# Performance work log

Measured on AMD Instinct MI355X. Metric: run time of the kernel, lower is better.

The kernel has to match this reference:

```python
import jax, jax.numpy as jnp
import numpy as np
from jax import lax


def _conv_block(x, w, b):
    # conv5x5 stride1 VALID + bias, ReLU, maxpool 2x2 stride 2 (NCHW)
    y = lax.conv_general_dilated(x, w, (1, 1), 'VALID',
                                 dimension_numbers=('NCHW', 'OIHW', 'NCHW'))
    y = jax.nn.relu(y + b[None, :, None, None])
    return lax.reduce_window(y, -np.inf, lax.max, (1, 1, 2, 2), (1, 1, 2, 2), 'VALID')


def _attention(feat, g, w, b):
    # feat: [B,C,H,W]; g: [B,512]; Linear(512 -> C)
    q = g @ w.T + b  # [B,C]
    Bn, C, H, W = feat.shape
    f = feat.reshape(Bn, C, H * W)
    # compat_scores[b,n] = sum_c f[b,c,n] * q[b,c] ; softmax over spatial dim
    a = jax.nn.softmax(jnp.einsum('bcn,bc->bn', f, q), axis=1)
    # weighted sum over spatial locations -> [B,C]
    return jnp.einsum('bcn,bn->bc', f, a)


def setup_inputs() -> dict:
    key = jax.random.key(0)
    ks = jax.random.split(key, 12)
    s = 0.02
    f32 = jnp.float32
    return {
        'x': jax.random.normal(ks[0], (16, 1, 220, 220), f32),
        'w1': jax.random.normal(ks[1], (64, 1, 5, 5), f32) * s,
        'b1': jnp.zeros((64,), f32),
        'w2': jax.random.normal(ks[2], (128, 64, 5, 5), f32) * s,
        'b2': jnp.zeros((128,), f32),
        'w3': jax.random.normal(ks[3], (256, 128, 5, 5), f32) * s,
        'b3': jnp.zeros((256,), f32),
        'fcw': jax.random.normal(ks[4], (512, 256 * 24 * 24), f32) * 0.002,
        'fcb': jnp.zeros((512,), f32),
        'aw1': jax.random.normal(ks[5], (64, 512), f32) * s,
        'ab1': jnp.zeros((64,), f32),
        'aw2': jax.random.normal(ks[6], (128, 512), f32) * s,
        'ab2': jnp.zeros((128,), f32),
        'aw3': jax.random.normal(ks[7], (256, 512), f32) * s,
        'ab3': jnp.zeros((256,), f32),
    }


def reference(x, w1, b1, w2, b2, w3, b3, fcw, fcb, aw1, ab1, aw2, ab2, aw3, ab3):
    o1 = _conv_block(x, w1, b1)    # [B,64,108,108]
    o2 = _conv_block(o1, w2, b2)   # [B,128,52,52]
    o3 = _conv_block(o2, w3, b3)   # [B,256,24,24]
    # dropout layers are identity at inference
    flat = o3.reshape(o3.shape[0], -1)          # [B, 256*24*24]
    g = flat @ fcw.T + fcb                       # [B, 512]
    att1 = _attention(o1, g, aw1, ab1)           # [B, 64]
    att2 = _attention(o2, g, aw2, ab2)           # [B, 128]
    att3 = _attention(o3, g, aw3, ab3)           # [B, 256]
    return jnp.concatenate([att1, att2, att3], axis=1)  # [B, 448]
```

## Files before the change

kernel.cpp:

```cpp
#include <hip/hip_runtime.h>
#include <cstdint>

typedef __attribute__((ext_vector_type(8))) short short8;
typedef __attribute__((ext_vector_type(4))) float f32x4;

__device__ __forceinline__ ushort f2bf(float f) {
  union { float f; uint32_t u; } v; v.f = f;
  uint32_t u = v.u;
  return (ushort)((u + 0x7fffu + ((u >> 16) & 1u)) >> 16);
}
__device__ __forceinline__ float bf2f(ushort h) {
  union { uint32_t u; float f; } v; v.u = ((uint32_t)h) << 16;
  return v.f;
}

__global__ __launch_bounds__(256) void prelude_k(
    const float* __restrict__ x, const float* __restrict__ w1, const float* __restrict__ b1,
    const float* __restrict__ w2, const float* __restrict__ w3,
    ushort* __restrict__ o1, ushort* __restrict__ w2t, ushort* __restrict__ w3t,
    float* __restrict__ g, float* __restrict__ out) {
  __shared__ ushort sb[28 * 29];
  const int tid = threadIdx.x;
  const int bx = blockIdx.x;
  if (bx >= 1296) {
    if (bx < 4496) {
      int idx = (bx - 1296) * 256 + tid;
      if (idx < 204800) {
        int j = idx & 7, lane = (idx >> 3) & 63, ks = (idx >> 9) & 1,
            fo = (idx >> 10) & 7, kpos = idx >> 13;
        int oc = fo * 16 + (lane & 15);
        int ic = ks * 32 + (lane >> 4) * 8 + j;
        w2t[idx] = f2bf(w2[((size_t)oc * 64 + ic) * 25 + kpos]);
      }
      {
        int j = idx & 7, lane = (idx >> 3) & 63, ks = (idx >> 9) & 3,
            fo = (idx >> 11) & 15, kpos = idx >> 15;
        int oc = fo * 16 + (lane & 15);
        int ic = ks * 32 + (lane >> 4) * 8 + j;
        w3t[idx] = f2bf(w3[((size_t)oc * 128 + ic) * 25 + kpos]);
      }
    } else {
      for (int i = tid; i < 8192; i += 256) g[i] = 0.f;
      for (int i = tid; i < 7168; i += 256) out[i] = 0.f;
    }
    return;
  }
  const int b = bx / 81, rem = bx % 81, ty = rem / 9, tx = rem % 9;
  for (int i = tid; i < 784; i += 256) {
    int iy = i / 28, ix = i % 28;
    sb[iy * 29 + ix] = f2bf(x[((size_t)b * 220 + ty * 24 + iy) * 220 + tx * 24 + ix]);
  }
  __syncthreads();
  const int lane = tid & 63, wid = tid >> 6;
  const int m16 = lane & 15, qd = lane >> 4;
  short8 bfr[4];
#pragma unroll
  for (int n = 0; n < 4; n++) {
    union { ushort u[8]; short8 v; } t;
#pragma unroll
    for (int j = 0; j < 8; j++) {
      int k = qd * 8 + j;
      int kc = k < 25 ? k : 0;
      ushort val = f2bf(w1[(n * 16 + m16) * 25 + kc]);
      t.u[j] = (k < 25) ? val : (ushort)0;
    }
    bfr[n] = t.v;
  }
  int offs[8];
#pragma unroll
  for (int j = 0; j < 8; j++) {
    int k = qd * 8 + j;
    int kc = k < 25 ? k : 24;
    offs[j] = (kc / 5) * 29 + (kc % 5);
  }
  float bias[4];
#pragma unroll
  for (int n = 0; n < 4; n++) bias[n] = b1[n * 16 + m16];
  for (int gg = 0; gg < 9; gg++) {
    int gr = wid * 9 + gg;
    int wglob = gr * 4 + (m16 >> 2);
    int wy = wglob / 12, wx = wglob % 12;
    int py = wy * 2 + ((m16 >> 1) & 1), px = wx * 2 + (m16 & 1);
    int base = py * 29 + px;
    union { ushort u[8]; short8 v; } a;
#pragma unroll
    for (int j = 0; j < 8; j++) a.u[j] = sb[base + offs[j]];
    int wgd = gr * 4 + qd;
    int gy = ty * 12 + wgd / 12, gx = tx * 12 + wgd % 12;
    size_t oidx = (((size_t)b * 108 + gy) * 108 + gx) * 64;
#pragma unroll
    for (int n = 0; n < 4; n++) {
      f32x4 d = (f32x4){0.f, 0.f, 0.f, 0.f};
      d = __builtin_amdgcn_mfma_f32_16x16x32_bf16(a.v, bfr[n], d, 0, 0, 0);
      float mx = fmaxf(fmaxf(d[0], d[1]), fmaxf(d[2], d[3]));
      o1[oidx + n * 16 + m16] = f2bf(fmaxf(mx + bias[n], 0.f));
    }
  }
}

template <int IC, int ICP, int OCT, int OCB, int INW, int POOLW>
__global__ __launch_bounds__(256) void conv_mfma(const ushort* __restrict__ in,
                                                 const ushort* __restrict__ wt,
                                                 const float* __restrict__ bias,
                                                 ushort* __restrict__ out) {
  constexpr int NPIX = 144;
  constexpr int PSTRIDE = OCB + 8;
  constexpr int LDSA = 2 * NPIX * ICP;
  constexpr int LDSP = 2 * 64 * PSTRIDE;
  constexpr int LDSN = (LDSA > LDSP) ? LDSA : LDSP;
  constexpr int NKS = IC / 32;
  constexpr int NFRAG = OCT / 16;
  __shared__ ushort sm[LDSN];
  const int tid = threadIdx.x;
  const int wid = tid >> 6, lane = tid & 63;
  const int m16 = lane & 15, qd = lane >> 4;
  const int bh = wid >> 1, og = wid & 1;
  constexpr int OCSPLIT = OCT / OCB;
  const int bpair = blockIdx.z / OCSPLIT;
  const int ocblk = (blockIdx.z % OCSPLIT) * OCB;
  const int b0 = bpair * 2;
  const int ty = blockIdx.y, tx = blockIdx.x;
  {
    constexpr int C8 = IC / 8;
    for (int i = tid; i < 2 * NPIX * C8; i += 256) {
      int bb = i / (NPIX * C8), rem = i % (NPIX * C8);
      int px = rem / C8, c8 = rem % C8;
      int gy = ty * 8 + px / 12, gx = tx * 8 + px % 12;
      uint4 v = *(const uint4*)(in + (((size_t)(b0 + bb) * INW + gy) * INW + gx) * IC + c8 * 8);
      *(uint4*)&sm[(bb * NPIX + px) * ICP + c8 * 8] = v;
    }
  }
  __syncthreads();
  f32x4 acc[4][4];
#pragma unroll
  for (int i = 0; i < 4; i++)
#pragma unroll
    for (int j = 0; j < 4; j++) acc[i][j] = (f32x4){0.f, 0.f, 0.f, 0.f};
  int aoff[4];
#pragma unroll
  for (int ms = 0; ms < 4; ms++) {
    int p = ms * 16 + m16;
    aoff[ms] = (bh * NPIX + (p >> 3) * 12 + (p & 7)) * ICP + qd * 8;
  }
  const int fo0 = (ocblk >> 4) + og * 4;
  for (int ky = 0; ky < 5; ky++) {
#pragma unroll
    for (int kx = 0; kx < 5; kx++) {
      const int koff = (ky * 12 + kx) * ICP;
      const ushort* wkp = wt + (((size_t)(ky * 5 + kx) * NFRAG + fo0) * NKS) * 512 + lane * 8;
#pragma unroll
      for (int ks = 0; ks < NKS; ks++) {
        short8 afr[4], bfr[4];
#pragma unroll
        for (int ms = 0; ms < 4; ms++)
          afr[ms] = *(const short8*)&sm[aoff[ms] + koff + ks * 32];
#pragma unroll
        for (int ns = 0; ns < 4; ns++)
          bfr[ns] = *(const short8*)(wkp + (ns * NKS + ks) * 512);
#pragma unroll
        for (int ms = 0; ms < 4; ms++)
#pragma unroll
          for (int ns = 0; ns < 4; ns++)
            acc[ms][ns] = __builtin_amdgcn_mfma_f32_16x16x32_bf16(afr[ms], bfr[ns], acc[ms][ns], 0, 0, 0);
      }
    }
  }
  __syncthreads();
#pragma unroll
  for (int ms = 0; ms < 4; ms++)
#pragma unroll
    for (int ns = 0; ns < 4; ns++) {
      int ocl = og * 64 + ns * 16 + m16;
      float bv = bias[ocblk + ocl];
#pragma unroll
      for (int r = 0; r < 4; r++) {
        int p = ms * 16 + qd * 4 + r;
        sm[(bh * 64 + p) * PSTRIDE + ocl] = f2bf(fmaxf(acc[ms][ns][r] + bv, 0.f));
      }
    }
  __syncthreads();
  constexpr int OC2 = OCB / 2;
  const int oc2 = tid % OC2, pst = tid / OC2;
  for (int pp = pst; pp < 32; pp += 256 / OC2) {
    int bb = pp >> 4, pl = pp & 15;
    int ppy = pl >> 2, ppx = pl & 3;
    int p00 = (ppy * 2) * 8 + ppx * 2;
    int oc = oc2 * 2;
    int base = bb * 64 * PSTRIDE;
    uint32_t v0 = *(const uint32_t*)&sm[base + p00 * PSTRIDE + oc];
    uint32_t v1 = *(const uint32_t*)&sm[base + (p00 + 1) * PSTRIDE + oc];
    uint32_t v2 = *(const uint32_t*)&sm[base + (p00 + 8) * PSTRIDE + oc];
    uint32_t v3 = *(const uint32_t*)&sm[base + (p00 + 9) * PSTRIDE + oc];
    float a0 = fmaxf(fmaxf(bf2f(v0 & 0xffff), bf2f(v1 & 0xffff)),
                     fmaxf(bf2f(v2 & 0xffff), bf2f(v3 & 0xffff)));
    float a1 = fmaxf(fmaxf(bf2f(v0 >> 16), bf2f(v1 >> 16)),
                     fmaxf(bf2f(v2 >> 16), bf2f(v3 >> 16)));
    uint32_t packed = ((uint32_t)f2bf(a1) << 16) | (uint32_t)f2bf(a0);
    int gy = ty * 4 + ppy, gx = tx * 4 + ppx;
    *(uint32_t*)&out[(((size_t)(b0 + bb) * POOLW + gy) * POOLW + gx) * OCT + ocblk + oc] = packed;
  }
}

__global__ void transpose_o3(const ushort* __restrict__ o3, ushort* __restrict__ flatT) {
  __shared__ ushort t[32][33];
  const int b = blockIdx.z;
  const int n0 = blockIdx.x * 32, c0 = blockIdx.y * 32;
  const int tid = threadIdx.x;
  {
    int cl = tid & 31, r = tid >> 5;
    for (int i = 0; i < 4; i++) {
      int nl = r + i * 8;
      t[nl][cl] = o3[((size_t)b * 576 + n0 + nl) * 256 + c0 + cl];
    }
  }
  __syncthreads();
  {
    int nl = tid & 31, r = tid >> 5;
    for (int i = 0; i < 4; i++) {
      int cl = r + i * 8;
      flatT[(size_t)b * 147456 + (c0 + cl) * 576 + n0 + nl] = t[nl][cl];
    }
  }
}

__global__ void fc_mfma(const ushort* __restrict__ flatT, const float* __restrict__ fcw,
                        float* __restrict__ g) {
  const int tid = threadIdx.x;
  const int wid = tid >> 6, lane = tid & 63;
  const int m16 = lane & 15, qd = lane >> 4;
  const int jt = blockIdx.y * 256 + wid * 64;
  const int K0 = blockIdx.x * 576;
  f32x4 acc[4];
#pragma unroll
  for (int f = 0; f < 4; f++) acc[f] = (f32x4){0.f, 0.f, 0.f, 0.f};
  const ushort* ap = flatT + (size_t)m16 * 147456 + K0 + qd * 8;
  const float* bp = fcw + (size_t)(jt + m16) * 147456 + K0 + qd * 8;
#pragma unroll 2
  for (int ks = 0; ks < 18; ks++) {
    short8 a = *(const short8*)(ap + ks * 32);
#pragma unroll
    for (int f = 0; f < 4; f++) {
      const float* bpf = bp + (size_t)f * 16 * 147456 + ks * 32;
      float4 b0 = *(const float4*)bpf;
      float4 b1 = *(const float4*)(bpf + 4);
      short8 bb;
      bb[0] = (short)f2bf(b0.x); bb[1] = (short)f2bf(b0.y);
      bb[2] = (short)f2bf(b0.z); bb[3] = (short)f2bf(b0.w);
      bb[4] = (short)f2bf(b1.x); bb[5] = (short)f2bf(b1.y);
      bb[6] = (short)f2bf(b1.z); bb[7] = (short)f2bf(b1.w);
      acc[f] = __builtin_amdgcn_mfma_f32_16x16x32_bf16(a, bb, acc[f], 0, 0, 0);
    }
  }
  const int brow = qd * 4;
#pragma unroll
  for (int f = 0; f < 4; f++)
#pragma unroll
    for (int r = 0; r < 4; r++)
      atomicAdd(&g[(brow + r) * 512 + jt + f * 16 + m16], acc[f][r]);
}

__global__ __launch_bounds__(256) void qcalc(const float* __restrict__ g,
                                             const float* __restrict__ fcb,
                                             const float* __restrict__ aw1, const float* __restrict__ ab1,
                                             const float* __restrict__ aw2, const float* __restrict__ ab2,
                                             const float* __restrict__ aw3, const float* __restrict__ ab3,
                                             float* __restrict__ q) {
  const int b = blockIdx.x, tid = threadIdx.x;
  __shared__ float gs[512];
  for (int i = tid; i < 512; i += 256) gs[i] = g[b * 512 + i] + fcb[i];
  __syncthreads();
  for (int c = tid; c < 448; c += 256) {
    const float* ar;
    float acc;
    if (c < 64)       { ar = aw1 + (size_t)c * 512;         acc = ab1[c]; }
    else if (c < 192) { ar = aw2 + (size_t)(c - 64) * 512;  acc = ab2[c - 64]; }
    else              { ar = aw3 + (size_t)(c - 192) * 512; acc = ab3[c - 192]; }
#pragma unroll 4
    for (int j = 0; j < 512; j += 4) {
      float4 a4 = *(const float4*)(ar + j);
      acc += a4.x * gs[j] + a4.y * gs[j + 1] + a4.z * gs[j + 2] + a4.w * gs[j + 3];
    }
    q[b * 448 + c] = acc;
  }
}

template <int C, int COFF>
__device__ __forceinline__ void score_head(const ushort* __restrict__ f,
                                           const float* __restrict__ q,
                                           float* __restrict__ s, int N, int nblk, int b,
                                           float* sq) {
  const int tid = threadIdx.x;
  if (tid < C) sq[tid] = q[b * 448 + COFF + tid];
  __syncthreads();
  int n = nblk * 256 + tid;
  if (n >= N) return;
  const ushort* fr = f + ((size_t)b * N + n) * C;
  float acc = 0.f;
#pragma unroll
  for (int c0 = 0; c0 < C; c0 += 8) {
    uint4 v = *(const uint4*)&fr[c0];
    uint32_t arr[4] = {v.x, v.y, v.z, v.w};
#pragma unroll
    for (int k = 0; k < 4; k++) {
      acc += bf2f(arr[k] & 0xffff) * sq[c0 + 2 * k];
      acc += bf2f(arr[k] >> 16) * sq[c0 + 2 * k + 1];
    }
  }
  s[(size_t)b * N + n] = acc;
}

__global__ void scores_all(const ushort* __restrict__ o1, const ushort* __restrict__ o2,
                           const ushort* __restrict__ o3, const float* __restrict__ q,
                           float* __restrict__ s1, float* __restrict__ s2,
                           float* __restrict__ s3) {
  __shared__ float sq[256];
  const int bx = blockIdx.x, b = blockIdx.y;
  if (bx < 46)      score_head<64, 0>(o1, q, s1, 11664, bx, b, sq);
  else if (bx < 57) score_head<128, 64>(o2, q, s2, 2704, bx - 46, b, sq);
  else              score_head<256, 192>(o3, q, s3, 576, bx - 57, b, sq);
}

__global__ void stats_all(const float* __restrict__ s1, const float* __restrict__ s2,
                          const float* __restrict__ s3, float* __restrict__ st) {
  const int b = blockIdx.x, head = blockIdx.y, tid = threadIdx.x;
  const float* s; int N; float* stp;
  if (head == 0)      { s = s1; N = 11664; stp = st; }
  else if (head == 1) { s = s2; N = 2704;  stp = st + 32; }
  else                { s = s3; N = 576;   stp = st + 64; }
  const float* sb = s + (size_t)b * N;
  __shared__ float red[4];
  float m = -1e30f;
  for (int i = tid; i < N; i += 256) m = fmaxf(m, sb[i]);
  for (int o = 32; o; o >>= 1) m = fmaxf(m, __shfl_xor(m, o));
  if ((tid & 63) == 0) red[tid >> 6] = m;
  __syncthreads();
  m = fmaxf(fmaxf(red[0], red[1]), fmaxf(red[2], red[3]));
  __syncthreads();
  float l = 0.f;
  for (int i = tid; i < N; i += 256) l += __expf(sb[i] - m);
  for (int o = 32; o; o >>= 1) l += __shfl_xor(l, o);
  if ((tid & 63) == 0) red[tid >> 6] = l;
  __syncthreads();
  if (tid == 0) { stp[b * 2] = m; stp[b * 2 + 1] = red[0] + red[1] + red[2] + red[3]; }
}

template <int C, int COFF, int CHUNK>
__device__ __forceinline__ void wsum_head(const ushort* __restrict__ f,
                                          const float* __restrict__ s,
                                          const float* __restrict__ st,
                                          float* __restrict__ out, int N, int nblk, int b) {
  const int tid = threadIdx.x;
  constexpr int S = 256 / C;
  const int c = tid % C, sub = tid / C;
  const float m = st[b * 2], rl = 1.f / st[b * 2 + 1];
  const float* sb = s + (size_t)b * N;
  const ushort* fb = f + (size_t)b * N * C;
  int n0 = nblk * CHUNK;
  int n1 = n0 + CHUNK; if (n1 > N) n1 = N;
  float acc = 0.f;
  for (int n = n0 + sub; n < n1; n += S) {
    float w = __expf(sb[n] - m);
    acc += w * bf2f(fb[(size_t)n * C + c]);
  }
  atomicAdd(&out[b * 448 + COFF + c], acc * rl);
}

__global__ void wsum_all(const ushort* __restrict__ o1, const ushort* __restrict__ o2,
                         const ushort* __restrict__ o3, const float* __restrict__ s1,
                         const float* __restrict__ s2, const float* __restrict__ s3,
                         const float* __restrict__ st, float* __restrict__ out) {
  const int bx = blockIdx.x, b = blockIdx.y;
  if (bx < 24)      wsum_head<64, 0, 486>(o1, s1, st, out, 11664, bx, b);
  else if (bx < 40) wsum_head<128, 64, 169>(o2, s2, st + 32, out, 2704, bx - 24, b);
  else              wsum_head<256, 192, 72>(o3, s3, st + 64, out, 576, bx - 40, b);
}

extern "C" void kernel_launch(void* const* d_in, const int* in_sizes, int n_in,
                              void* d_out, int out_size, void* d_ws, size_t ws_size,
                              hipStream_t stream) {
  const float* x   = (const float*)d_in[0];
  const float* w1  = (const float*)d_in[1];
  const float* b1  = (const float*)d_in[2];
  const float* w2  = (const float*)d_in[3];
  const float* b2  = (const float*)d_in[4];
  const float* w3  = (const float*)d_in[5];
  const float* b3  = (const float*)d_in[6];
  const float* fcw = (const float*)d_in[7];
  const float* fcb = (const float*)d_in[8];
  const float* aw1 = (const float*)d_in[9];
  const float* ab1 = (const float*)d_in[10];
  const float* aw2 = (const float*)d_in[11];
  const float* ab2 = (const float*)d_in[12];
  const float* aw3 = (const float*)d_in[13];
  const float* ab3 = (const float*)d_in[14];
  float* out = (float*)d_out;
  char* ws = (char*)d_ws;

  ushort* o1    = (ushort*)(ws + 0);
  ushort* o2    = (ushort*)(ws + 23887872);
  ushort* o3    = (ushort*)(ws + 34963456);
  ushort* flatT = (ushort*)(ws + 39682048);
  ushort* w2t   = (ushort*)(ws + 44400640);
  ushort* w3t   = (ushort*)(ws + 44810240);
  float*  g     = (float*)(ws + 46448640);
  float*  s1    = (float*)(ws + 46510080);
  float*  s2    = (float*)(ws + 47256576);
  float*  s3    = (float*)(ws + 47429632);
  float*  st    = (float*)(ws + 47466496);
  float*  q     = (float*)(ws + 47466880);

  prelude_k<<<4497, 256, 0, stream>>>(x, w1, b1, w2, w3, o1, w2t, w3t, g, out);
  conv_mfma<64, 72, 128, 128, 108, 52><<<dim3(13, 13, 8), 256, 0, stream>>>(o1, w2t, b2, o2);
  conv_mfma<128, 136, 256, 128, 52, 24><<<dim3(6, 6, 16), 256, 0, stream>>>(o2, w3t, b3, o3);
  transpose_o3<<<dim3(18, 8, 16), 256, 0, stream>>>(o3, flatT);
  fc_mfma<<<dim3(256, 2), 256, 0, stream>>>(flatT, fcw, g);
  qcalc<<<16, 256, 0, stream>>>(g, fcb, aw1, ab1, aw2, ab2, aw3, ab3, q);
  scores_all<<<dim3(60, 16), 256, 0, stream>>>(o1, o2, o3, q, s1, s2, s3);
  stats_all<<<dim3(16, 3), 256, 0, stream>>>(s1, s2, s3, st);
  wsum_all<<<dim3(48, 16), 256, 0, stream>>>(o1, o2, o3, s1, s2, s3, st, out);
}
```

Baseline: 710.8 us.

## Retile conv3 over all output channels, split FC and qcalc finer, stage wsum weights

The conv kernel is now templated on warps per output-channel group. For conv3, one block covers all 256 output channels of a single image, so each input tile is loaded once rather than once per 128-channel half, and launch bounds ask for 3 blocks per CU. The FC K-split gets smaller chunks and more blocks, and qcalc is split over two channel halves for more parallelism. wsum now computes exp weights once into LDS, reads bf16 pairs, and reduces through shared atomics before the global atomic, cutting redundant exp work and global atomics at the cost of extra syncs and LDS.

```diff
diff --git a/kernel.cpp b/kernel.cpp
--- a/kernel.cpp
+++ b/kernel.cpp
@@ -98,15 +98,16 @@
   }
 }
 
-template <int IC, int ICP, int OCT, int OCB, int INW, int POOLW>
-__global__ __launch_bounds__(256) void conv_mfma(const ushort* __restrict__ in,
-                                                 const ushort* __restrict__ wt,
-                                                 const float* __restrict__ bias,
-                                                 ushort* __restrict__ out) {
+template <int IC, int ICP, int OCT, int WOC, int INW, int POOLW>
+__global__ __launch_bounds__(256, 3) void conv_mfma(const ushort* __restrict__ in,
+                                                    const ushort* __restrict__ wt,
+                                                    const float* __restrict__ bias,
+                                                    ushort* __restrict__ out) {
+  constexpr int NB = 4 / WOC;
   constexpr int NPIX = 144;
-  constexpr int PSTRIDE = OCB + 8;
-  constexpr int LDSA = 2 * NPIX * ICP;
-  constexpr int LDSP = 2 * 64 * PSTRIDE;
+  constexpr int PSTRIDE = OCT + 8;
+  constexpr int LDSA = NB * NPIX * ICP;
+  constexpr int LDSP = NB * 64 * PSTRIDE;
   constexpr int LDSN = (LDSA > LDSP) ? LDSA : LDSP;
   constexpr int NKS = IC / 32;
   constexpr int NFRAG = OCT / 16;
@@ -114,15 +115,12 @@
   const int tid = threadIdx.x;
   const int wid = tid >> 6, lane = tid & 63;
   const int m16 = lane & 15, qd = lane >> 4;
-  const int bh = wid >> 1, og = wid & 1;
-  constexpr int OCSPLIT = OCT / OCB;
-  const int bpair = blockIdx.z / OCSPLIT;
-  const int ocblk = (blockIdx.z % OCSPLIT) * OCB;
-  const int b0 = bpair * 2;
+  const int bh = wid / WOC, og = wid % WOC;
+  const int b0 = blockIdx.z * NB;
   const int ty = blockIdx.y, tx = blockIdx.x;
   {
     constexpr int C8 = IC / 8;
-    for (int i = tid; i < 2 * NPIX * C8; i += 256) {
+    for (int i = tid; i < NB * NPIX * C8; i += 256) {
       int bb = i / (NPIX * C8), rem = i % (NPIX * C8);
       int px = rem / C8, c8 = rem % C8;
       int gy = ty * 8 + px / 12, gx = tx * 8 + px % 12;
@@ -142,7 +140,7 @@
     int p = ms * 16 + m16;
     aoff[ms] = (bh * NPIX + (p >> 3) * 12 + (p & 7)) * ICP + qd * 8;
   }
-  const int fo0 = (ocblk >> 4) + og * 4;
+  const int fo0 = og * 4;
   for (int ky = 0; ky < 5; ky++) {
 #pragma unroll
     for (int kx = 0; kx < 5; kx++) {
@@ -171,7 +169,7 @@
 #pragma unroll
     for (int ns = 0; ns < 4; ns++) {
       int ocl = og * 64 + ns * 16 + m16;
-      float bv = bias[ocblk + ocl];
+      float bv = bias[ocl];
 #pragma unroll
       for (int r = 0; r < 4; r++) {
         int p = ms * 16 + qd * 4 + r;
@@ -179,9 +177,9 @@
       }
     }
   __syncthreads();
-  constexpr int OC2 = OCB / 2;
+  constexpr int OC2 = OCT / 2;
   const int oc2 = tid % OC2, pst = tid / OC2;
-  for (int pp = pst; pp < 32; pp += 256 / OC2) {
+  for (int pp = pst; pp < NB * 16; pp += 256 / OC2) {
     int bb = pp >> 4, pl = pp & 15;
     int ppy = pl >> 2, ppx = pl & 3;
     int p00 = (ppy * 2) * 8 + ppx * 2;
@@ -197,7 +195,7 @@
                      fmaxf(bf2f(v2 >> 16), bf2f(v3 >> 16)));
     uint32_t packed = ((uint32_t)f2bf(a1) << 16) | (uint32_t)f2bf(a0);
     int gy = ty * 4 + ppy, gx = tx * 4 + ppx;
-    *(uint32_t*)&out[(((size_t)(b0 + bb) * POOLW + gy) * POOLW + gx) * OCT + ocblk + oc] = packed;
+    *(uint32_t*)&out[(((size_t)(b0 + bb) * POOLW + gy) * POOLW + gx) * OCT + oc] = packed;
   }
 }
 
@@ -229,14 +227,14 @@
   const int wid = tid >> 6, lane = tid & 63;
   const int m16 = lane & 15, qd = lane >> 4;
   const int jt = blockIdx.y * 256 + wid * 64;
-  const int K0 = blockIdx.x * 576;
+  const int K0 = blockIdx.x * 384;
   f32x4 acc[4];
 #pragma unroll
   for (int f = 0; f < 4; f++) acc[f] = (f32x4){0.f, 0.f, 0.f, 0.f};
   const ushort* ap = flatT + (size_t)m16 * 147456 + K0 + qd * 8;
   const float* bp = fcw + (size_t)(jt + m16) * 147456 + K0 + qd * 8;
 #pragma unroll 2
-  for (int ks = 0; ks < 18; ks++) {
+  for (int ks = 0; ks < 12; ks++) {
     short8 a = *(const short8*)(ap + ks * 32);
 #pragma unroll
     for (int f = 0; f < 4; f++) {
@@ -266,10 +264,11 @@
                                              const float* __restrict__ aw3, const float* __restrict__ ab3,
                                              float* __restrict__ q) {
   const int b = blockIdx.x, tid = threadIdx.x;
+  const int cpart = blockIdx.y;
   __shared__ float gs[512];
   for (int i = tid; i < 512; i += 256) gs[i] = g[b * 512 + i] + fcb[i];
   __syncthreads();
-  for (int c = tid; c < 448; c += 256) {
+  for (int c = cpart * 224 + tid; c < cpart * 224 + 224; c += 256) {
     const float* ar;
     float acc;
     if (c < 64)       { ar = aw1 + (size_t)c * 512;         acc = ab1[c]; }
@@ -348,31 +347,44 @@
 __device__ __forceinline__ void wsum_head(const ushort* __restrict__ f,
                                           const float* __restrict__ s,
                                           const float* __restrict__ st,
-                                          float* __restrict__ out, int N, int nblk, int b) {
-  const int tid = threadIdx.x;
-  constexpr int S = 256 / C;
-  const int c = tid % C, sub = tid / C;
+                                          float* __restrict__ out, int N, int nblk, int b,
+                                          float* ws, float* os) {
+  const int tid = threadIdx.x;
   const float m = st[b * 2], rl = 1.f / st[b * 2 + 1];
   const float* sb = s + (size_t)b * N;
   const ushort* fb = f + (size_t)b * N * C;
-  int n0 = nblk * CHUNK;
+  const int n0 = nblk * CHUNK;
   int n1 = n0 + CHUNK; if (n1 > N) n1 = N;
-  float acc = 0.f;
-  for (int n = n0 + sub; n < n1; n += S) {
-    float w = __expf(sb[n] - m);
-    acc += w * bf2f(fb[(size_t)n * C + c]);
-  }
-  atomicAdd(&out[b * 448 + COFF + c], acc * rl);
+  const int L = n1 - n0;
+  for (int i = tid; i < L; i += 256) ws[i] = __expf(sb[n0 + i] - m);
+  for (int i = tid; i < C; i += 256) os[i] = 0.f;
+  __syncthreads();
+  constexpr int C2 = C / 2;
+  constexpr int S2 = 256 / C2;
+  const int c2 = tid % C2, sub = tid / C2;
+  float a0 = 0.f, a1 = 0.f;
+  for (int i = sub; i < L; i += S2) {
+    uint32_t v = *(const uint32_t*)&fb[(size_t)(n0 + i) * C + c2 * 2];
+    float w = ws[i];
+    a0 += w * bf2f(v & 0xffff);
+    a1 += w * bf2f(v >> 16);
+  }
+  atomicAdd(&os[c2 * 2], a0);
+  atomicAdd(&os[c2 * 2 + 1], a1);
+  __syncthreads();
+  for (int i = tid; i < C; i += 256) atomicAdd(&out[b * 448 + COFF + i], os[i] * rl);
 }
 
 __global__ void wsum_all(const ushort* __restrict__ o1, const ushort* __restrict__ o2,
                          const ushort* __restrict__ o3, const float* __restrict__ s1,
                          const float* __restrict__ s2, const float* __restrict__ s3,
                          const float* __restrict__ st, float* __restrict__ out) {
+  __shared__ float ws[488];
+  __shared__ float os[256];
   const int bx = blockIdx.x, b = blockIdx.y;
-  if (bx < 24)      wsum_head<64, 0, 486>(o1, s1, st, out, 11664, bx, b);
-  else if (bx < 40) wsum_head<128, 64, 169>(o2, s2, st + 32, out, 2704, bx - 24, b);
-  else              wsum_head<256, 192, 72>(o3, s3, st + 64, out, 576, bx - 40, b);
+  if (bx < 24)      wsum_head<64, 0, 486>(o1, s1, st, out, 11664, bx, b, ws, os);
+  else if (bx < 40) wsum_head<128, 64, 169>(o2, s2, st + 32, out, 2704, bx - 24, b, ws, os);
+  else              wsum_head<256, 192, 72>(o3, s3, st + 64, out, 576, bx - 40, b, ws, os);
 }
 
 extern "C" void kernel_launch(void* const* d_in, const int* in_sizes, int n_in,
@@ -410,11 +422,11 @@
   float*  q     = (float*)(ws + 47466880);
 
   prelude_k<<<4497, 256, 0, stream>>>(x, w1, b1, w2, w3, o1, w2t, w3t, g, out);
-  conv_mfma<64, 72, 128, 128, 108, 52><<<dim3(13, 13, 8), 256, 0, stream>>>(o1, w2t, b2, o2);
-  conv_mfma<128, 136, 256, 128, 52, 24><<<dim3(6, 6, 16), 256, 0, stream>>>(o2, w3t, b3, o3);
+  conv_mfma<64, 72, 128, 2, 108, 52><<<dim3(13, 13, 8), 256, 0, stream>>>(o1, w2t, b2, o2);
+  conv_mfma<128, 136, 256, 4, 52, 24><<<dim3(6, 6, 16), 256, 0, stream>>>(o2, w3t, b3, o3);
   transpose_o3<<<dim3(18, 8, 16), 256, 0, stream>>>(o3, flatT);
-  fc_mfma<<<dim3(256, 2), 256, 0, stream>>>(flatT, fcw, g);
-  qcalc<<<16, 256, 0, stream>>>(g, fcb, aw1, ab1, aw2, ab2, aw3, ab3, q);
+  fc_mfma<<<dim3(384, 2), 256, 0, stream>>>(flatT, fcw, g);
+  qcalc<<<dim3(16, 2), 256, 0, stream>>>(g, fcb, aw1, ab1, aw2, ab2, aw3, ab3, q);
   scores_all<<<dim3(60, 16), 256, 0, stream>>>(o1, o2, o3, q, s1, s2, s3);
   stats_all<<<dim3(16, 3), 256, 0, stream>>>(s1, s2, s3, st);
   wsum_all<<<dim3(48, 16), 256, 0, stream>>>(o1, o2, o3, s1, s2, s3, st, out);
```

Result: faster. 652.0 us (-8.3%).
